# Performance work log

Measured on AMD Instinct MI355X. Metric: run time of the kernel, lower is better.

The kernel has to match this reference:

```python
import jax, jax.numpy as jnp
import numpy as np

N, M, T_STEPS = 32, 64, 20000  # t = T/dt = 200/0.01
DT = 0.01
SQRT_DT = DT ** 0.5


def setup_inputs() -> dict:
    key = jax.random.key(0)
    k1, k2 = jax.random.split(key)
    # theta ~ U(lower, upper) per the module's prior (4-param variant)
    lower = jnp.array([0.5, 0.1, 0.1, 0.0], dtype=jnp.float32)
    upper = jnp.array([1.5, 3.0, 0.6, 4.0], dtype=jnp.float32)
    theta = lower + (upper - lower) * jax.random.uniform(k1, (N, 4), dtype=jnp.float32)
    noise = jax.random.normal(k2, (N, M, T_STEPS), dtype=jnp.float32)
    return {"theta": theta, "noise": noise}


def reference(theta, noise):
    # Euler-Maruyama OU recurrence: x_{i+1} = x_i + gamma*(mu - x_i)*dt + sigma*sqrt(dt)*eps_i
    n, m, t = noise.shape
    gamma = theta[:, 0][:, None]  # [n,1] broadcasts over m
    mu = theta[:, 1][:, None]
    sigma = theta[:, 2][:, None]
    x0 = jnp.broadcast_to(theta[:, 3][:, None], (n, m))

    eps_t = jnp.moveaxis(noise, -1, 0)  # [t, n, m] for scan

    def step(x, eps):
        x_new = x + gamma * (mu - x) * DT + sigma * SQRT_DT * eps
        return x_new, x_new

    _, xs = jax.lax.scan(step, x0, eps_t)  # xs: [t, n, m] == x[:, :, 1:]
    return jnp.moveaxis(xs, 0, -1)  # [n, m, t]
```

## Files before the change

### kernel.cpp

```cpp
#include <hip/hip_runtime.h>


#define T_STEPS 20000
#define M_PATHS 64
#define CHUNK   8
#define TILE    (64 * CHUNK)
#define NTILES  ((T_STEPS + TILE - 1) / TILE)
#define DT      0.01f
#define SQRT_DT 0.1f

__global__ __launch_bounds__(256) void ou_scan_kernel(
    const float* __restrict__ theta,
    const float* __restrict__ noise,
    float* __restrict__ out)
{
    const int wave  = threadIdx.x >> 6;
    const int lane  = threadIdx.x & 63;
    const int chain = blockIdx.x * 4 + wave;
    const int n     = chain / M_PATHS;

    const float gamma = theta[n * 4 + 0];
    const float mu    = theta[n * 4 + 1];
    const float sigma = theta[n * 4 + 2];
    float carry       = theta[n * 4 + 3];

    const float a    = 1.0f - gamma * DT;
    const float gmdt = gamma * mu * DT;
    const float ssd  = sigma * SQRT_DT;
    const float a2 = a * a;
    const float a4 = a2 * a2;
    const float a8 = a4 * a4;

    const float* __restrict__ np_ = noise + (size_t)chain * T_STEPS;
    float* __restrict__       op_ = out   + (size_t)chain * T_STEPS;

    float4 c0 = make_float4(0.f, 0.f, 0.f, 0.f);
    float4 c1 = make_float4(0.f, 0.f, 0.f, 0.f);
    {
        const int e0 = lane * CHUNK;
        if (e0 + CHUNK <= T_STEPS) {
            c0 = *(const float4*)(np_ + e0);
            c1 = *(const float4*)(np_ + e0 + 4);
        }
    }

    for (int tb = 0; tb < NTILES; ++tb) {
        float4 n0 = make_float4(0.f, 0.f, 0.f, 0.f);
        float4 n1 = make_float4(0.f, 0.f, 0.f, 0.f);
        const int ne0 = (tb + 1) * TILE + lane * CHUNK;
        if (tb + 1 < NTILES && ne0 + CHUNK <= T_STEPS) {
            n0 = *(const float4*)(np_ + ne0);
            n1 = *(const float4*)(np_ + ne0 + 4);
        }

        const int  base = tb * TILE + lane * CHUNK;
        const bool cact = (base + CHUNK <= T_STEPS);

        const float b0 = fmaf(ssd, c0.x, gmdt);
        const float b1 = fmaf(ssd, c0.y, gmdt);
        const float b2 = fmaf(ssd, c0.z, gmdt);
        const float b3 = fmaf(ssd, c0.w, gmdt);
        const float b4 = fmaf(ssd, c1.x, gmdt);
        const float b5 = fmaf(ssd, c1.y, gmdt);
        const float b6 = fmaf(ssd, c1.z, gmdt);
        const float b7 = fmaf(ssd, c1.w, gmdt);

        float p = b0;
        p = fmaf(p, a, b1);
        p = fmaf(p, a, b2);
        p = fmaf(p, a, b3);
        p = fmaf(p, a, b4);
        p = fmaf(p, a, b5);
        p = fmaf(p, a, b6);
        p = fmaf(p, a, b7);

        float A = cact ? a8 : 1.0f;
        float B = cact ? p  : 0.0f;

        #pragma unroll
        for (int d = 1; d < 64; d <<= 1) {
            const float pA = __shfl_up(A, d);
            const float pB = __shfl_up(B, d);
            if (lane >= d) {
                B = fmaf(A, pB, B);
                A = A * pA;
            }
        }

        float Aex = __shfl_up(A, 1);
        float Bex = __shfl_up(B, 1);
        if (lane == 0) { Aex = 1.0f; Bex = 0.0f; }
        float x = fmaf(Aex, carry, Bex);

        const float A63 = __shfl(A, 63);
        const float B63 = __shfl(B, 63);
        carry = fmaf(A63, carry, B63);

        if (cact) {
            float4 o0, o1;
            x = fmaf(a, x, b0); o0.x = x;
            x = fmaf(a, x, b1); o0.y = x;
            x = fmaf(a, x, b2); o0.z = x;
            x = fmaf(a, x, b3); o0.w = x;
            x = fmaf(a, x, b4); o1.x = x;
            x = fmaf(a, x, b5); o1.y = x;
            x = fmaf(a, x, b6); o1.z = x;
            x = fmaf(a, x, b7); o1.w = x;
            *(float4*)(op_ + base)     = o0;
            *(float4*)(op_ + base + 4) = o1;
        }

        c0 = n0;
        c1 = n1;
    }
}

extern "C" void kernel_launch(void* const* d_in, const int* in_sizes, int n_in,
                              void* d_out, int out_size, void* d_ws, size_t ws_size,
                              hipStream_t stream) {
    const float* theta = (const float*)d_in[0];
    const float* noise = (const float*)d_in[1];
    float* out = (float*)d_out;

    const int chains = in_sizes[1] / T_STEPS;
    const int blocks = chains / 4;
    ou_scan_kernel<<<blocks, 256, 0, stream>>>(theta, noise, out);
}
```

Before: 289.9 us.

## Split each chain's scan across four waves with LDS cross-wave combine

Each OU chain now runs on a whole 256-thread block instead of a single wave, so every block-tile covers 2048 time steps and the serial tile loop runs about four times fewer iterations. Per-wave scan totals go to double-buffered shared memory and are combined after a __syncthreads to get each wave's prefix and the carry into the next tile. The grid grows from 512 to 2048 blocks, which raises the number of waves per chain, at the cost of one block barrier and a short LDS reduction per tile. The first noise load now runs without a bounds check, which relies on T_STEPS being at least 2048.

```diff
diff --git a/kernel.cpp b/kernel.cpp
--- a/kernel.cpp
+++ b/kernel.cpp
@@ -4,20 +4,25 @@
 #define T_STEPS 20000
 #define M_PATHS 64
 #define CHUNK   8
-#define TILE    (64 * CHUNK)
-#define NTILES  ((T_STEPS + TILE - 1) / TILE)
+#define NWAVES  4
+#define BLOCK   (NWAVES * 64)
+#define BTILE   (BLOCK * CHUNK)
+#define NBT     ((T_STEPS + BTILE - 1) / BTILE)
 #define DT      0.01f
 #define SQRT_DT 0.1f
 
-__global__ __launch_bounds__(256) void ou_scan_kernel(
+__global__ __launch_bounds__(BLOCK, 8) void ou_scan_kernel(
     const float* __restrict__ theta,
     const float* __restrict__ noise,
     float* __restrict__ out)
 {
-    const int wave  = threadIdx.x >> 6;
-    const int lane  = threadIdx.x & 63;
-    const int chain = blockIdx.x * 4 + wave;
-    const int n     = chain / M_PATHS;
+    __shared__ float sA[2][NWAVES], sB[2][NWAVES];
+
+    const int tid   = threadIdx.x;
+    const int wave  = tid >> 6;
+    const int lane  = tid & 63;
+    const int chain = blockIdx.x;
+    const int n     = chain >> 6;
 
     const float gamma = theta[n * 4 + 0];
     const float mu    = theta[n * 4 + 1];
@@ -34,27 +39,24 @@
     const float* __restrict__ np_ = noise + (size_t)chain * T_STEPS;
     float* __restrict__       op_ = out   + (size_t)chain * T_STEPS;
 
-    float4 c0 = make_float4(0.f, 0.f, 0.f, 0.f);
-    float4 c1 = make_float4(0.f, 0.f, 0.f, 0.f);
+    float4 c0, c1;
     {
-        const int e0 = lane * CHUNK;
-        if (e0 + CHUNK <= T_STEPS) {
-            c0 = *(const float4*)(np_ + e0);
-            c1 = *(const float4*)(np_ + e0 + 4);
-        }
+        const int e0 = tid * CHUNK;
+        c0 = *(const float4*)(np_ + e0);
+        c1 = *(const float4*)(np_ + e0 + 4);
     }
 
-    for (int tb = 0; tb < NTILES; ++tb) {
+    for (int tb = 0; tb < NBT; ++tb) {
         float4 n0 = make_float4(0.f, 0.f, 0.f, 0.f);
         float4 n1 = make_float4(0.f, 0.f, 0.f, 0.f);
-        const int ne0 = (tb + 1) * TILE + lane * CHUNK;
-        if (tb + 1 < NTILES && ne0 + CHUNK <= T_STEPS) {
+        const int ne0 = (tb + 1) * BTILE + tid * CHUNK;
+        if (ne0 + CHUNK <= T_STEPS) {
             n0 = *(const float4*)(np_ + ne0);
             n1 = *(const float4*)(np_ + ne0 + 4);
         }
 
-        const int  base = tb * TILE + lane * CHUNK;
-        const bool cact = (base + CHUNK <= T_STEPS);
+        const int  base = tb * BTILE + tid * CHUNK;
+        const bool act  = (base + CHUNK <= T_STEPS);
 
         const float b0 = fmaf(ssd, c0.x, gmdt);
         const float b1 = fmaf(ssd, c0.y, gmdt);
@@ -74,8 +76,8 @@
         p = fmaf(p, a, b6);
         p = fmaf(p, a, b7);
 
-        float A = cact ? a8 : 1.0f;
-        float B = cact ? p  : 0.0f;
+        float A = act ? a8 : 1.0f;
+        float B = act ? p  : 0.0f;
 
         #pragma unroll
         for (int d = 1; d < 64; d <<= 1) {
@@ -87,16 +89,28 @@
             }
         }
 
+        if (lane == 63) { sA[tb & 1][wave] = A; sB[tb & 1][wave] = B; }
+        __syncthreads();
+
+        float PA = 1.f, PB = 0.f, FA = 1.f, FB = 0.f;
+        #pragma unroll
+        for (int w = 0; w < NWAVES; ++w) {
+            const float aw = sA[tb & 1][w];
+            const float bw = sB[tb & 1][w];
+            if (w < wave) { PB = fmaf(aw, PB, bw); PA *= aw; }
+            FB = fmaf(aw, FB, bw); FA *= aw;
+        }
+
+        const float xw = fmaf(PA, carry, PB);
+
         float Aex = __shfl_up(A, 1);
         float Bex = __shfl_up(B, 1);
-        if (lane == 0) { Aex = 1.0f; Bex = 0.0f; }
-        float x = fmaf(Aex, carry, Bex);
+        if (lane == 0) { Aex = 1.f; Bex = 0.f; }
+        float x = fmaf(Aex, xw, Bex);
 
-        const float A63 = __shfl(A, 63);
-        const float B63 = __shfl(B, 63);
-        carry = fmaf(A63, carry, B63);
+        carry = fmaf(FA, carry, FB);
 
-        if (cact) {
+        if (act) {
             float4 o0, o1;
             x = fmaf(a, x, b0); o0.x = x;
             x = fmaf(a, x, b1); o0.y = x;
@@ -123,6 +137,5 @@
     float* out = (float*)d_out;
 
     const int chains = in_sizes[1] / T_STEPS;
-    const int blocks = chains / 4;
-    ou_scan_kernel<<<blocks, 256, 0, stream>>>(theta, noise, out);
+    ou_scan_kernel<<<chains, BLOCK, 0, stream>>>(theta, noise, out);
 }
```

Result: no change. 288.8 us (-0.4%).
